# Kernel tuning notes

Hardware: AMD Instinct MI355X
Metric: run time of the kernel (lower is better)

## Reference

```python
import jax, jax.numpy as jnp
import numpy as np

EMBED_DIM = 1024
NUM_HEADS = 16
HEAD_DIM = EMBED_DIM // NUM_HEADS


def setup_inputs() -> dict:
    key = jax.random.key(0)
    ks = jax.random.split(key, 9)
    B, S, D = 4, 2048, EMBED_DIM
    s = 1.0 / np.sqrt(D)
    return {
        "x": jax.random.normal(ks[0], (B, S, D), dtype=jnp.float32),
        "Wq": jax.random.uniform(ks[1], (D, D), jnp.float32, -s, s),
        "bq": jax.random.uniform(ks[2], (D,), jnp.float32, -s, s),
        "Wk": jax.random.uniform(ks[3], (D, D), jnp.float32, -s, s),
        "bk": jax.random.uniform(ks[4], (D,), jnp.float32, -s, s),
        "Wv": jax.random.uniform(ks[5], (D, D), jnp.float32, -s, s),
        "bv": jax.random.uniform(ks[6], (D,), jnp.float32, -s, s),
        "Wo": jax.random.uniform(ks[7], (D, D), jnp.float32, -s, s),
        "bo": jax.random.uniform(ks[8], (D,), jnp.float32, -s, s),
    }


def reference(x, Wq, bq, Wk, bk, Wv, bv, Wo, bo):
    B, S, D = x.shape
    H, Hd = NUM_HEADS, HEAD_DIM

    def proj(W, b):
        # torch Linear: x @ W.T + b; reshape to [B, H, S, Hd]
        y = jnp.einsum('bsd,ed->bse', x, W) + b
        return y.reshape(B, S, H, Hd).transpose(0, 2, 1, 3)

    Q = proj(Wq, bq)
    K = proj(Wk, bk)
    V = proj(Wv, bv)
    scores = jnp.einsum('bhqd,bhkd->bhqk', Q, K) / np.sqrt(Hd).astype(jnp.float32)
    attn = jax.nn.softmax(scores, axis=-1)
    out = jnp.einsum('bhqk,bhkd->bhqd', attn, V)
    out = out.transpose(0, 2, 1, 3).reshape(B, S, D)
    return jnp.einsum('bsd,ed->bse', out, Wo) + bo
```

## Files before the change

kernel.cpp:

```cpp
#include <hip/hip_runtime.h>
#include <stdint.h>

typedef unsigned short u16;
typedef _Float16 f16;
typedef __fp16 fp16x2 __attribute__((ext_vector_type(2)));
typedef f16 f16x8 __attribute__((ext_vector_type(8)));
typedef float f32x4 __attribute__((ext_vector_type(4)));
typedef u16 u16x8v __attribute__((ext_vector_type(8)));

#define MFMAH __builtin_amdgcn_mfma_f32_16x16x32_f16

__device__ __forceinline__ void gload16(const void* g, void* l) {
    __builtin_amdgcn_global_load_lds(
        (const __attribute__((address_space(1))) uint32_t*)g,
        (__attribute__((address_space(3))) uint32_t*)l, 16, 0, 0);
}

__global__ __launch_bounds__(256) void convert_x(const float4* __restrict__ x,
                                                 f16x8* __restrict__ o) {
    int i = blockIdx.x * 256 + threadIdx.x;
    float4 a = x[2 * i], b = x[2 * i + 1];
    f16x8 h;
    h[0] = (f16)a.x; h[1] = (f16)a.y; h[2] = (f16)a.z; h[3] = (f16)a.w;
    h[4] = (f16)b.x; h[5] = (f16)b.y; h[6] = (f16)b.z; h[7] = (f16)b.w;
    o[i] = h;
}

__global__ __launch_bounds__(256) void convert_w(const float4* __restrict__ Wq,
                                                 const float4* __restrict__ Wk,
                                                 const float4* __restrict__ Wv,
                                                 const float4* __restrict__ Wo,
                                                 f16x8* __restrict__ hi,
                                                 f16x8* __restrict__ lo) {
    int gi = blockIdx.x * 256 + threadIdx.x;
    int wsel = gi >> 17;
    int li = gi & 131071;
    const float4* src = (wsel == 0) ? Wq : (wsel == 1) ? Wk : (wsel == 2) ? Wv : Wo;
    float4 a = src[2 * li], b = src[2 * li + 1];
    float v[8] = {a.x, a.y, a.z, a.w, b.x, b.y, b.z, b.w};
    f16x8 h;
#pragma unroll
    for (int j = 0; j < 8; ++j) h[j] = (f16)v[j];
    hi[gi] = h;
    if (wsel == 3) {
        f16x8 l;
#pragma unroll
        for (int j = 0; j < 8; ++j) l[j] = (f16)(v[j] - (float)h[j]);
        lo[gi] = l;
    }
}

__global__ __launch_bounds__(512, 4)
void gemm_qkv(const f16* __restrict__ A,
              const f16* __restrict__ Whi,
              const float* __restrict__ b0, const float* __restrict__ b1,
              const float* __restrict__ b2,
              f16* __restrict__ oq, f16* __restrict__ ok, f16* __restrict__ ov) {
    __shared__ f16 ldsA[256 * 64];
    __shared__ f16 ldsW[128 * 64];
    const int t = threadIdx.x;
    const int lane = t & 63, quad = lane >> 4, l16 = lane & 15;
    const int wid = t >> 6;
    const int wsel = blockIdx.x >> 3;
    const int bm = blockIdx.y * 256;
    const int bn = (blockIdx.x & 7) * 128;
    const int wm = (wid >> 1) * 64, wn = (wid & 1) * 64;
    const f16* Wh = Whi + (size_t)wsel * 1048576;
    const float* bias = (wsel == 0) ? b0 : (wsel == 1) ? b1 : b2;

    f32x4 acc[4][4] = {};

    for (int kt = 0; kt < 16; ++kt) {
        __syncthreads();
        const int k0 = kt * 64;
#pragma unroll
        for (int c = 0; c < 4; ++c) {
            const int u = c * 512 + t;
            const int r = u >> 3, cc = u & 7;
            const int sc = cc ^ (r & 7);
            gload16(A + (size_t)(bm + r) * 1024 + k0 + sc * 8, &ldsA[u * 8]);
        }
#pragma unroll
        for (int c = 0; c < 2; ++c) {
            const int u = c * 512 + t;
            const int r = u >> 3, cc = u & 7;
            const int sc = cc ^ (r & 7);
            gload16(Wh + (size_t)(bn + r) * 1024 + k0 + sc * 8, &ldsW[u * 8]);
        }
        __syncthreads();

#pragma unroll
        for (int kq = 0; kq < 2; ++kq) {
            f16x8 bh[4];
            const int chb = kq * 4 + quad;
            const int ch = chb ^ (l16 & 7);
#pragma unroll
            for (int i = 0; i < 4; ++i) {
                const int rb = wn + i * 16 + l16;
                bh[i] = *(const f16x8*)&ldsW[rb * 64 + ch * 8];
            }
#pragma unroll
            for (int mi = 0; mi < 4; ++mi) {
                const int ra = wm + mi * 16 + l16;
                const f16x8 af = *(const f16x8*)&ldsA[ra * 64 + ch * 8];
#pragma unroll
                for (int ni = 0; ni < 4; ++ni)
                    acc[mi][ni] = MFMAH(af, bh[ni], acc[mi][ni], 0, 0, 0);
            }
        }
    }

#pragma unroll
    for (int ni = 0; ni < 4; ++ni) {
        const int e = bn + wn + ni * 16 + l16;
        const float bv = bias[e];
        const int h = e >> 6, d = e & 63;
#pragma unroll
        for (int mi = 0; mi < 4; ++mi) {
            const int row0 = bm + wm + mi * 16 + quad * 4;
            if (wsel == 2) {
                const int b = row0 >> 11, s0 = row0 & 2047;
                ushort4 pk;
                f16 p0 = (f16)(acc[mi][ni][0] + bv);
                f16 p1 = (f16)(acc[mi][ni][1] + bv);
                f16 p2 = (f16)(acc[mi][ni][2] + bv);
                f16 p3 = (f16)(acc[mi][ni][3] + bv);
                pk.x = __builtin_bit_cast(u16, p0);
                pk.y = __builtin_bit_cast(u16, p1);
                pk.z = __builtin_bit_cast(u16, p2);
                pk.w = __builtin_bit_cast(u16, p3);
                *(ushort4*)(ov + ((size_t)((b * 16 + h) * 64 + d)) * 2048 + s0) = pk;
            } else {
                f16* dst = (wsel == 0) ? oq : ok;
#pragma unroll
                for (int r = 0; r < 4; ++r) {
                    const int row = row0 + r;
                    const int b = row >> 11, s = row & 2047;
                    float v = acc[mi][ni][r] + bv;
                    if (wsel == 0) v *= 0.18033688f;
                    dst[((size_t)((b * 16 + h) * 2048 + s)) * 64 + d] = (f16)v;
                }
            }
        }
    }
}

__global__ __launch_bounds__(256, 2)
void gemm_o(const f16* __restrict__ A,
            const f16* __restrict__ Wh, const f16* __restrict__ Wl,
            const float* __restrict__ bias, float* __restrict__ ofp) {
    __shared__ f16 ldsA[128 * 64];
    __shared__ f16 ldsW[2][128 * 64];
    const int t = threadIdx.x;
    const int lane = t & 63, quad = lane >> 4, l16 = lane & 15;
    const int wid = t >> 6;
    const int bm = blockIdx.y * 128, bn = blockIdx.x * 128;
    const int wm = (wid >> 1) * 64, wn = (wid & 1) * 64;

    f32x4 acc[4][4] = {};

    for (int kt = 0; kt < 16; ++kt) {
        __syncthreads();
        const int k0 = kt * 64;
#pragma unroll
        for (int c = 0; c < 4; ++c) {
            const int u = c * 256 + t;
            const int r = u >> 3, cc = u & 7;
            const int sc = cc ^ (r & 7);
            gload16(A + (size_t)(bm + r) * 1024 + k0 + sc * 8, &ldsA[u * 8]);
        }
#pragma unroll
        for (int p = 0; p < 2; ++p) {
            const f16* Ws = p ? Wl : Wh;
#pragma unroll
            for (int c = 0; c < 4; ++c) {
                const int u = c * 256 + t;
                const int r = u >> 3, cc = u & 7;
                const int sc = cc ^ (r & 7);
                gload16(Ws + (size_t)(bn + r) * 1024 + k0 + sc * 8, &ldsW[p][u * 8]);
            }
        }
        __syncthreads();

#pragma unroll
        for (int kq = 0; kq < 2; ++kq) {
            f16x8 bh[4], bl[4];
            const int ch = (kq * 4 + quad) ^ (l16 & 7);
#pragma unroll
            for (int i = 0; i < 4; ++i) {
                const int rb = wn + i * 16 + l16;
                bh[i] = *(const f16x8*)&ldsW[0][rb * 64 + ch * 8];
                bl[i] = *(const f16x8*)&ldsW[1][rb * 64 + ch * 8];
            }
#pragma unroll
            for (int mi = 0; mi < 4; ++mi) {
                const int ra = wm + mi * 16 + l16;
                const f16x8 af = *(const f16x8*)&ldsA[ra * 64 + ch * 8];
#pragma unroll
                for (int ni = 0; ni < 4; ++ni) {
                    acc[mi][ni] = MFMAH(af, bh[ni], acc[mi][ni], 0, 0, 0);
                    acc[mi][ni] = MFMAH(af, bl[ni], acc[mi][ni], 0, 0, 0);
                }
            }
        }
    }

#pragma unroll
    for (int ni = 0; ni < 4; ++ni) {
        const int e = bn + wn + ni * 16 + l16;
        const float bv = bias[e];
#pragma unroll
        for (int mi = 0; mi < 4; ++mi) {
            const int row0 = bm + wm + mi * 16 + quad * 4;
#pragma unroll
            for (int r = 0; r < 4; ++r)
                ofp[(size_t)(row0 + r) * 1024 + e] = acc[mi][ni][r] + bv;
        }
    }
}

__global__ __launch_bounds__(256, 2)
void attn_fused(const f16* __restrict__ Q, const f16* __restrict__ K,
                const f16* __restrict__ Vt, f16* __restrict__ AO) {
    __shared__ f16 Kt[128 * 64];
    __shared__ f16 Vs[64 * 128];
    __shared__ f16 Pw[4][4][16 * 50];
    const int t = threadIdx.x, wid = t >> 6, lane = t & 63;
    const int quad = lane >> 4, l16 = lane & 15;
    const int sw7 = l16 & 7;
    const int bh = blockIdx.x;
    const int q0 = blockIdx.y * 256;
    const size_t base = (size_t)bh * (2048 * 64);

    const u16x8v ou = {0x3C00, 0x3C00, 0x3C00, 0x3C00, 0x3C00, 0x3C00, 0x3C00, 0x3C00};
    const f16x8 ONES = __builtin_bit_cast(f16x8, ou);

    f16x8 qf[4][2];
#pragma unroll
    for (int s = 0; s < 4; ++s) {
        const int qrow = q0 + wid * 64 + s * 16 + l16;
        qf[s][0] = *(const f16x8*)(Q + base + (size_t)qrow * 64 + quad * 8);
        qf[s][1] = *(const f16x8*)(Q + base + (size_t)qrow * 64 + 32 + quad * 8);
    }

    f32x4 of[4][4] = {};
    f32x4 rs[4] = {};

    for (int kt = 0; kt < 16; ++kt) {
        __syncthreads();
#pragma unroll
        for (int c = 0; c < 4; ++c) {
            const int u = c * 256 + t;
            const int row = u >> 3, cc = u & 7;
            const int sc = cc ^ (row & 7);
            gload16(K + base + (size_t)(kt * 128 + row) * 64 + sc * 8, &Kt[u * 8]);
        }
#pragma unroll
        for (int c = 0; c < 4; ++c) {
            const int u = c * 256 + t;
            const int row = u >> 4, cc = u & 15;
            const int sc = cc ^ (row & 15);
            gload16(Vt + base + (size_t)row * 2048 + kt * 128 + sc * 8, &Vs[u * 8]);
        }
        __syncthreads();

#pragma unroll
        for (int kk = 0; kk < 4; ++kk) {
#pragma unroll
            for (int nn = 0; nn < 2; ++nn) {
                const int row = (kk * 2 + nn) * 16 + l16;
                const f16x8 kb0 = *(const f16x8*)&Kt[row * 64 + (quad ^ sw7) * 8];
                const f16x8 kb1 = *(const f16x8*)&Kt[row * 64 + ((4 | quad) ^ sw7) * 8];
#pragma unroll
                for (int s = 0; s < 4; ++s) {
                    f32x4 sf = {};
                    sf = MFMAH(kb0, qf[s][0], sf, 0, 0, 0);
                    sf = MFMAH(kb1, qf[s][1], sf, 0, 0, 0);
                    const float p0 = __builtin_amdgcn_exp2f(sf[0]);
                    const float p1 = __builtin_amdgcn_exp2f(sf[1]);
                    const float p2 = __builtin_amdgcn_exp2f(sf[2]);
                    const float p3 = __builtin_amdgcn_exp2f(sf[3]);
                    const fp16x2 d0 = __builtin_amdgcn_cvt_pkrtz(p0, p1);
                    const fp16x2 d1 = __builtin_amdgcn_cvt_pkrtz(p2, p3);
                    uint32_t* pp = (uint32_t*)&Pw[wid][s][l16 * 50 + nn * 16 + quad * 4];
                    pp[0] = __builtin_bit_cast(uint32_t, d0);
                    pp[1] = __builtin_bit_cast(uint32_t, d1);
                }
            }
            f16x8 pf[4];
#pragma unroll
            for (int s = 0; s < 4; ++s)
                pf[s] = *(const f16x8*)&Pw[wid][s][l16 * 50 + quad * 8];
#pragma unroll
            for (int di = 0; di < 4; ++di) {
                const int row = di * 16 + l16;
                const f16x8 vb = *(const f16x8*)&Vs[row * 128 + ((kk * 4 + quad) ^ l16) * 8];
#pragma unroll
                for (int s = 0; s < 4; ++s)
                    of[s][di] = MFMAH(vb, pf[s], of[s][di], 0, 0, 0);
            }
#pragma unroll
            for (int s = 0; s < 4; ++s)
                rs[s] = MFMAH(ONES, pf[s], rs[s], 0, 0, 0);
        }
    }

    const int b = bh >> 4, h = bh & 15;
#pragma unroll
    for (int s = 0; s < 4; ++s) {
        const int qrow = q0 + wid * 64 + s * 16 + l16;
        const float inv = 1.0f / rs[s][0];
#pragma unroll
        for (int di = 0; di < 4; ++di) {
            const int e0 = h * 64 + di * 16 + quad * 4;
            ushort4 pk;
            f16 o0 = (f16)(of[s][di][0] * inv);
            f16 o1 = (f16)(of[s][di][1] * inv);
            f16 o2 = (f16)(of[s][di][2] * inv);
            f16 o3 = (f16)(of[s][di][3] * inv);
            pk.x = __builtin_bit_cast(u16, o0);
            pk.y = __builtin_bit_cast(u16, o1);
            pk.z = __builtin_bit_cast(u16, o2);
            pk.w = __builtin_bit_cast(u16, o3);
            *(ushort4*)(AO + (size_t)(b * 2048 + qrow) * 1024 + e0) = pk;
        }
    }
}

extern "C" void kernel_launch(void* const* d_in, const int* in_sizes, int n_in,
                              void* d_out, int out_size, void* d_ws, size_t ws_size,
                              hipStream_t stream) {
    const float* x  = (const float*)d_in[0];
    const float* Wq = (const float*)d_in[1];
    const float* bq = (const float*)d_in[2];
    const float* Wk = (const float*)d_in[3];
    const float* bk = (const float*)d_in[4];
    const float* Wv = (const float*)d_in[5];
    const float* bv = (const float*)d_in[6];
    const float* Wo = (const float*)d_in[7];
    const float* bo = (const float*)d_in[8];
    float* out = (float*)d_out;

    char* ws = (char*)d_ws;
    f16* XF  = (f16*)(ws);
    f16* WH  = (f16*)(ws + (16u << 20));
    f16* WL  = (f16*)(ws + (24u << 20));
    f16* QF  = (f16*)(ws + (32u << 20));
    f16* KF  = (f16*)(ws + (48u << 20));
    f16* VTF = (f16*)(ws + (64u << 20));
    f16* AOF = (f16*)(ws + (80u << 20));

    convert_x<<<4096, 256, 0, stream>>>((const float4*)x, (f16x8*)XF);
    convert_w<<<2048, 256, 0, stream>>>((const float4*)Wq, (const float4*)Wk,
                                        (const float4*)Wv, (const float4*)Wo,
                                        (f16x8*)WH, (f16x8*)WL);

    gemm_qkv<<<dim3(24, 32), 512, 0, stream>>>(XF, WH, bq, bk, bv, QF, KF, VTF);

    attn_fused<<<dim3(64, 8), 256, 0, stream>>>(QF, KF, VTF, AOF);

    gemm_o<<<dim3(8, 64), 256, 0, stream>>>(AOF, WH + 3145728, WL + 3145728, bo, out);
}
```

Baseline: 277.3 us.

## Halve attention query tile and move P transpose from LDS to bpermute

The attention kernel now processes 128 query rows per block instead of 256, with 32 per wave, and launches twice as many blocks with a launch bound allowing 4 blocks per CU. The per-wave P staging buffer in shared memory is removed. The exp'd scores are instead redistributed into the MFMA B-operand layout with ds_bpermute cross-lane shuffles. This cuts LDS footprint and register pressure to raise occupancy and parallelism, but each K/V tile is now loaded by twice as many blocks, and the shuffles add instructions.

```diff
diff --git a/kernel.cpp b/kernel.cpp
--- a/kernel.cpp
+++ b/kernel.cpp
@@ -7,6 +7,7 @@
 typedef f16 f16x8 __attribute__((ext_vector_type(8)));
 typedef float f32x4 __attribute__((ext_vector_type(4)));
 typedef u16 u16x8v __attribute__((ext_vector_type(8)));
+typedef uint32_t u32x4 __attribute__((ext_vector_type(4)));
 
 #define MFMAH __builtin_amdgcn_mfma_f32_16x16x32_f16
 
@@ -219,32 +220,35 @@
     }
 }
 
-__global__ __launch_bounds__(256, 2)
+__global__ __launch_bounds__(256, 4)
 void attn_fused(const f16* __restrict__ Q, const f16* __restrict__ K,
                 const f16* __restrict__ Vt, f16* __restrict__ AO) {
     __shared__ f16 Kt[128 * 64];
     __shared__ f16 Vs[64 * 128];
-    __shared__ f16 Pw[4][4][16 * 50];
     const int t = threadIdx.x, wid = t >> 6, lane = t & 63;
     const int quad = lane >> 4, l16 = lane & 15;
     const int sw7 = l16 & 7;
     const int bh = blockIdx.x;
-    const int q0 = blockIdx.y * 256;
+    const int q0 = blockIdx.y * 128;
     const size_t base = (size_t)bh * (2048 * 64);
 
     const u16x8v ou = {0x3C00, 0x3C00, 0x3C00, 0x3C00, 0x3C00, 0x3C00, 0x3C00, 0x3C00};
     const f16x8 ONES = __builtin_bit_cast(f16x8, ou);
 
-    f16x8 qf[4][2];
-#pragma unroll
-    for (int s = 0; s < 4; ++s) {
-        const int qrow = q0 + wid * 64 + s * 16 + l16;
+    const int idxA = (((quad & 1) << 5) + l16) << 2;
+    const int idxB = idxA + 64;
+    const bool loPlane = quad < 2;
+
+    f16x8 qf[2][2];
+#pragma unroll
+    for (int s = 0; s < 2; ++s) {
+        const int qrow = q0 + wid * 32 + s * 16 + l16;
         qf[s][0] = *(const f16x8*)(Q + base + (size_t)qrow * 64 + quad * 8);
         qf[s][1] = *(const f16x8*)(Q + base + (size_t)qrow * 64 + 32 + quad * 8);
     }
 
-    f32x4 of[4][4] = {};
-    f32x4 rs[4] = {};
+    f32x4 of[2][4] = {};
+    f32x4 rs[2] = {};
 
     for (int kt = 0; kt < 16; ++kt) {
         __syncthreads();
@@ -266,13 +270,14 @@
 
 #pragma unroll
         for (int kk = 0; kk < 4; ++kk) {
+            int xp[2][2][2];
 #pragma unroll
             for (int nn = 0; nn < 2; ++nn) {
                 const int row = (kk * 2 + nn) * 16 + l16;
                 const f16x8 kb0 = *(const f16x8*)&Kt[row * 64 + (quad ^ sw7) * 8];
                 const f16x8 kb1 = *(const f16x8*)&Kt[row * 64 + ((4 | quad) ^ sw7) * 8];
 #pragma unroll
-                for (int s = 0; s < 4; ++s) {
+                for (int s = 0; s < 2; ++s) {
                     f32x4 sf = {};
                     sf = MFMAH(kb0, qf[s][0], sf, 0, 0, 0);
                     sf = MFMAH(kb1, qf[s][1], sf, 0, 0, 0);
@@ -280,35 +285,46 @@
                     const float p1 = __builtin_amdgcn_exp2f(sf[1]);
                     const float p2 = __builtin_amdgcn_exp2f(sf[2]);
                     const float p3 = __builtin_amdgcn_exp2f(sf[3]);
-                    const fp16x2 d0 = __builtin_amdgcn_cvt_pkrtz(p0, p1);
-                    const fp16x2 d1 = __builtin_amdgcn_cvt_pkrtz(p2, p3);
-                    uint32_t* pp = (uint32_t*)&Pw[wid][s][l16 * 50 + nn * 16 + quad * 4];
-                    pp[0] = __builtin_bit_cast(uint32_t, d0);
-                    pp[1] = __builtin_bit_cast(uint32_t, d1);
+                    xp[nn][s][0] = __builtin_bit_cast(int, __builtin_amdgcn_cvt_pkrtz(p0, p1));
+                    xp[nn][s][1] = __builtin_bit_cast(int, __builtin_amdgcn_cvt_pkrtz(p2, p3));
                 }
             }
-            f16x8 pf[4];
-#pragma unroll
-            for (int s = 0; s < 4; ++s)
-                pf[s] = *(const f16x8*)&Pw[wid][s][l16 * 50 + quad * 8];
+            f16x8 pf[2];
+#pragma unroll
+            for (int s = 0; s < 2; ++s) {
+                const int qa00 = __builtin_amdgcn_ds_bpermute(idxA, xp[0][s][0]);
+                const int qa01 = __builtin_amdgcn_ds_bpermute(idxA, xp[0][s][1]);
+                const int qa10 = __builtin_amdgcn_ds_bpermute(idxA, xp[1][s][0]);
+                const int qa11 = __builtin_amdgcn_ds_bpermute(idxA, xp[1][s][1]);
+                const int qb00 = __builtin_amdgcn_ds_bpermute(idxB, xp[0][s][0]);
+                const int qb01 = __builtin_amdgcn_ds_bpermute(idxB, xp[0][s][1]);
+                const int qb10 = __builtin_amdgcn_ds_bpermute(idxB, xp[1][s][0]);
+                const int qb11 = __builtin_amdgcn_ds_bpermute(idxB, xp[1][s][1]);
+                const uint32_t dw0 = (uint32_t)(loPlane ? qa00 : qa10);
+                const uint32_t dw1 = (uint32_t)(loPlane ? qa01 : qa11);
+                const uint32_t dw2 = (uint32_t)(loPlane ? qb00 : qb10);
+                const uint32_t dw3 = (uint32_t)(loPlane ? qb01 : qb11);
+                u32x4 pw = {dw0, dw1, dw2, dw3};
+                pf[s] = __builtin_bit_cast(f16x8, pw);
+            }
 #pragma unroll
             for (int di = 0; di < 4; ++di) {
                 const int row = di * 16 + l16;
                 const f16x8 vb = *(const f16x8*)&Vs[row * 128 + ((kk * 4 + quad) ^ l16) * 8];
 #pragma unroll
-                for (int s = 0; s < 4; ++s)
+                for (int s = 0; s < 2; ++s)
                     of[s][di] = MFMAH(vb, pf[s], of[s][di], 0, 0, 0);
             }
 #pragma unroll
-            for (int s = 0; s < 4; ++s)
+            for (int s = 0; s < 2; ++s)
                 rs[s] = MFMAH(ONES, pf[s], rs[s], 0, 0, 0);
         }
     }
 
     const int b = bh >> 4, h = bh & 15;
 #pragma unroll
-    for (int s = 0; s < 4; ++s) {
-        const int qrow = q0 + wid * 64 + s * 16 + l16;
+    for (int s = 0; s < 2; ++s) {
+        const int qrow = q0 + wid * 32 + s * 16 + l16;
         const float inv = 1.0f / rs[s][0];
 #pragma unroll
         for (int di = 0; di < 4; ++di) {
@@ -357,7 +373,7 @@
 
     gemm_qkv<<<dim3(24, 32), 512, 0, stream>>>(XF, WH, bq, bk, bv, QF, KF, VTF);
 
-    attn_fused<<<dim3(64, 8), 256, 0, stream>>>(QF, KF, VTF, AOF);
+    attn_fused<<<dim3(64, 16), 256, 0, stream>>>(QF, KF, VTF, AOF);
 
     gemm_o<<<dim3(8, 64), 256, 0, stream>>>(AOF, WH + 3145728, WL + 3145728, bo, out);
 }
```

Result: slower. 293.8 us (+6.0%).
